# Performance work log

Hardware: AMD Instinct MI355X
Metric: run time of the kernel (lower is better)

The kernel has to match this reference:

```python
import jax, jax.numpy as jnp
import numpy as np

D_MODEL, NUM_HEADS, ROPE_DIM = 256, 8, 16
B_GRAPHS, N_MAX = 16, 512


def _make_batch():
    # ragged graph sizes between 256 and 512 atoms; contiguous, sorted ids
    sizes = np.array([256 + (i * 256) // 15 for i in range(B_GRAPHS)], dtype=np.int64)
    return np.repeat(np.arange(B_GRAPHS), sizes)  # total N = 6137


def setup_inputs() -> dict:
    key = jax.random.key(0)
    ks = jax.random.split(key, 6)
    batch_np = _make_batch()
    N = int(batch_np.shape[0])
    x = jax.random.normal(ks[0], (N, D_MODEL), jnp.float32)
    pos = jax.random.normal(ks[1], (N, 3), jnp.float32) * 3.0
    W_qkv = jax.random.normal(ks[2], (D_MODEL, 3 * D_MODEL), jnp.float32) / np.sqrt(D_MODEL).astype(np.float32)
    W_out = jax.random.normal(ks[3], (D_MODEL, D_MODEL), jnp.float32) / np.sqrt(D_MODEL).astype(np.float32)
    rope_freqs = jax.random.normal(ks[4], (ROPE_DIM,), jnp.float32) * 0.1
    W_rope = jax.random.normal(ks[5], (ROPE_DIM, NUM_HEADS), jnp.float32) / np.sqrt(ROPE_DIM).astype(np.float32)
    gamma = jnp.ones((D_MODEL,), jnp.float32)
    beta = jnp.zeros((D_MODEL,), jnp.float32)
    return {"x": x, "pos": pos, "batch": jnp.asarray(batch_np, jnp.int32),
            "W_qkv": W_qkv, "W_out": W_out, "rope_freqs": rope_freqs,
            "W_rope": W_rope, "gamma": gamma, "beta": beta,
            "B": B_GRAPHS, "n_max": N_MAX}


def _forward(x, pos, W_qkv, W_out, rope_freqs, W_rope, gamma, beta, batch, B, n_max):
    N, d = x.shape
    H = W_rope.shape[1]
    hd = d // H
    scale = hd ** -0.5
    # pad ragged graphs to [B, n_max] via vectorized scatter (batch is sorted)
    sizes = jax.ops.segment_sum(jnp.ones((N,), jnp.int32), batch, num_segments=B)
    offsets = jnp.concatenate([jnp.zeros((1,), jnp.int32), jnp.cumsum(sizes)[:-1].astype(jnp.int32)])
    pidx = jnp.arange(N, dtype=jnp.int32) - offsets[batch]  # position within graph
    x_pad = jnp.zeros((B, n_max, d), x.dtype).at[batch, pidx].set(x)
    pos_pad = jnp.zeros((B, n_max, 3), pos.dtype).at[batch, pidx].set(pos)
    pad = jnp.ones((B, n_max), bool).at[batch, pidx].set(False)  # True = padding
    # multi-head self-attention on scalar channel
    qkv = x_pad @ W_qkv  # [B, n, 3d]
    q, k, v = jnp.split(qkv, 3, axis=-1)
    heads = lambda t: t.reshape(B, n_max, H, hd).transpose(0, 2, 1, 3)  # [B,H,n,hd]
    q, k, v = heads(q), heads(k), heads(v)
    logits = jnp.einsum('bhid,bhjd->bhij', q, k) * scale
    # Euclidean RoPE distance bias: rope_proj(cos(|omega| * ||r_i - r_j||))
    diff = pos_pad[:, :, None, :] - pos_pad[:, None, :, :]  # [B,n,n,3]
    sq = jnp.sum(diff * diff, axis=-1)
    dist = jnp.where(sq > 0, jnp.sqrt(jnp.where(sq > 0, sq, 1.0)), 0.0)  # safe norm
    fourier = jnp.cos(dist[..., None] * jnp.abs(rope_freqs))  # [B,n,n,r]
    bias = jnp.einsum('bijr,rh->bhij', fourier, W_rope)
    pair_pad = (pad[:, :, None] | pad[:, None, :])[:, None]  # [B,1,n,n]
    bias = jnp.where(pair_pad, 0.0, bias)
    logits = jnp.where(pad[:, None, None, :], -1e9, logits + bias)
    attn = jax.nn.softmax(logits, axis=-1)
    out = jnp.einsum('bhij,bhjd->bhid', attn, v)
    out = out.transpose(0, 2, 1, 3).reshape(B, n_max, d) @ W_out
    out_flat = out[batch, pidx]  # gather back to flat node list
    # residual + LayerNorm (eps = 1e-5)
    y = x + out_flat
    mu = jnp.mean(y, axis=-1, keepdims=True)
    var = jnp.mean((y - mu) ** 2, axis=-1, keepdims=True)
    return gamma * (y - mu) * jax.lax.rsqrt(var + 1e-5) + beta


def reference(x, pos, batch, W_qkv, W_out, rope_freqs, W_rope, gamma, beta, B, n_max):
    return _forward(x, pos, W_qkv, W_out, rope_freqs, W_rope, gamma, beta, batch, B, n_max)
```

## Files before the change

### kernel.cpp

```cpp
#include <hip/hip_runtime.h>
#include <hip/hip_bf16.h>

typedef __hip_bfloat16 bf16;
typedef short bf16x8 __attribute__((ext_vector_type(8)));
typedef float f32x4 __attribute__((ext_vector_type(4)));

#define NGRAPH 16
#define QSCALE 0.17677669529663687f
#define VT_LD 8192

struct __align__(16) bf8x { bf16 v[8]; };

__device__ __forceinline__ float b2f(bf16 v) { return __bfloat162float(v); }

__device__ __forceinline__ bf16x8 ldcvt8(const float* p) {
  float4 u = *(const float4*)p, v = *(const float4*)(p + 4);
  __align__(16) bf16 tmp[8];
  tmp[0] = __float2bfloat16(u.x); tmp[1] = __float2bfloat16(u.y);
  tmp[2] = __float2bfloat16(u.z); tmp[3] = __float2bfloat16(u.w);
  tmp[4] = __float2bfloat16(v.x); tmp[5] = __float2bfloat16(v.y);
  tmp[6] = __float2bfloat16(v.z); tmp[7] = __float2bfloat16(v.w);
  return *(const bf16x8*)tmp;
}

__global__ __launch_bounds__(256) void k_pre(const float* __restrict__ Wqkv,
                                             const float* __restrict__ Wout,
                                             const int* __restrict__ batch,
                                             const float* __restrict__ freqs,
                                             const float* __restrict__ Wrope,
                                             bf16* __restrict__ Wqkv_t,
                                             bf16* __restrict__ Wout_t,
                                             float* __restrict__ Tblg,
                                             int* __restrict__ offs, int N) {
  __shared__ float ld[64][65];
  int bid = blockIdx.x, t = threadIdx.x;
  int c = t & 63, r0 = t >> 6;
  if (bid < 48) {
    int k0 = (bid & 3) * 64, n0 = (bid >> 2) * 64;
    #pragma unroll
    for (int r = r0; r < 64; r += 4) ld[r][c] = Wqkv[(size_t)(k0 + r) * 768 + n0 + c];
    __syncthreads();
    #pragma unroll
    for (int r = r0; r < 64; r += 4)
      Wqkv_t[(size_t)(n0 + r) * 256 + k0 + c] = __float2bfloat16(ld[c][r]);
  } else if (bid < 64) {
    int b2 = bid - 48;
    int k0 = (b2 & 3) * 64, n0 = (b2 >> 2) * 64;
    #pragma unroll
    for (int r = r0; r < 64; r += 4) ld[r][c] = Wout[(size_t)(k0 + r) * 256 + n0 + c];
    __syncthreads();
    #pragma unroll
    for (int r = r0; r < 64; r += 4)
      Wout_t[(size_t)(n0 + r) * 256 + k0 + c] = __float2bfloat16(ld[c][r]);
  } else if (bid == 64) {
    for (int i = t; i < N; i += 256) {
      if (i == 0) { offs[0] = 0; offs[NGRAPH] = N; }
      else if (batch[i] != batch[i - 1]) offs[batch[i]] = i;
    }
  } else {
    int i = (bid - 65) * 256 + t;
    if (i < 384) {
      float d = i * 0.125f;
      float a[8];
      #pragma unroll
      for (int h = 0; h < 8; ++h) a[h] = 0.f;
      #pragma unroll
      for (int r = 0; r < 16; ++r) {
        float cv = __cosf(d * fabsf(freqs[r]));
        #pragma unroll
        for (int h = 0; h < 8; ++h) a[h] += cv * Wrope[r * 8 + h];
      }
      #pragma unroll
      for (int h = 0; h < 8; ++h) Tblg[i * 8 + h] = a[h];
    }
  }
}

__global__ __launch_bounds__(256) void k_gemm(const float* __restrict__ x,
                                              const bf16* __restrict__ Wqkv_t,
                                              const int* __restrict__ batch,
                                              const int* __restrict__ offs,
                                              bf16* __restrict__ QKVb,
                                              bf16* __restrict__ VT, int N) {
  __shared__ float tr[64][33];
  __shared__ int rowcol[32];
  int t = threadIdx.x;
  int w = t >> 6, l = t & 63, fr = l & 15, fq = l >> 4;
  int rh = w & 1, ch = w >> 1;
  int m0 = blockIdx.x * 32, n0 = blockIdx.y * 64;
  if (t < 32) {
    int m = m0 + t; if (m > N - 1) m = N - 1;
    int b = batch[m];
    rowcol[t] = b * 512 + (m - offs[b]);
  }
  int arow = m0 + rh * 16 + fr; if (arow > N - 1) arow = N - 1;
  bf16x8 af[8];
  #pragma unroll
  for (int kt = 0; kt < 8; ++kt)
    af[kt] = ldcvt8(x + (size_t)arow * 256 + kt * 32 + fq * 8);
  #pragma unroll
  for (int p = 0; p < 3; ++p) {
    f32x4 acc[2];
    #pragma unroll
    for (int nt = 0; nt < 2; ++nt) {
      acc[nt] = (f32x4){0.f, 0.f, 0.f, 0.f};
      int brow = p * 256 + n0 + ch * 32 + nt * 16 + fr;
      #pragma unroll
      for (int kt = 0; kt < 8; ++kt) {
        bf16x8 bf_ = *(const bf16x8*)(Wqkv_t + (size_t)brow * 256 + kt * 32 + fq * 8);
        acc[nt] = __builtin_amdgcn_mfma_f32_16x16x32_bf16(af[kt], bf_, acc[nt], 0, 0, 0);
      }
    }
    float sc = (p == 0) ? QSCALE : 1.f;
    #pragma unroll
    for (int nt = 0; nt < 2; ++nt) {
      int col = p * 256 + n0 + ch * 32 + nt * 16 + fr;
      #pragma unroll
      for (int rr = 0; rr < 4; ++rr) {
        int m = m0 + rh * 16 + fq * 4 + rr;
        if (m < N) QKVb[(size_t)m * 768 + col] = __float2bfloat16(acc[nt][rr] * sc);
      }
    }
    if (p == 2) {
      #pragma unroll
      for (int nt = 0; nt < 2; ++nt)
        #pragma unroll
        for (int rr = 0; rr < 4; ++rr)
          tr[ch * 32 + nt * 16 + fr][rh * 16 + fq * 4 + rr] = acc[nt][rr];
      __syncthreads();
      int c = t >> 2, rr0 = (t & 3) * 8;
      int dg = n0 + c;
      #pragma unroll
      for (int i = 0; i < 8; ++i) {
        int r = rr0 + i;
        VT[(size_t)dg * VT_LD + rowcol[r]] = __float2bfloat16(tr[c][r]);
      }
    }
  }
}

__global__ __launch_bounds__(256) void k_attn(const float* __restrict__ pos,
                                              const float* __restrict__ Tblg,
                                              const bf16* __restrict__ QKVb,
                                              const bf16* __restrict__ VT,
                                              const int* __restrict__ offs,
                                              float* __restrict__ Op,
                                              float* __restrict__ lp, int N, int JC) {
  __shared__ __align__(16) float Tgf[384][8];
  __shared__ __align__(16) bf16 Sbf[2][8][64][8];
  __shared__ __align__(16) bf16 Pt[4][16][40];
  int b = blockIdx.y, jc = blockIdx.z;
  int off = offs[b], n = offs[b + 1] - off;
  int q0 = blockIdx.x * 16;
  if (q0 >= n) return;
  int t = threadIdx.x, w = t >> 6, l = t & 63, fr = l & 15, fq = l >> 4;

  {
    float4* dst = (float4*)&Tgf[0][0];
    const float4* src = (const float4*)Tblg;
    #pragma unroll
    for (int i = t; i < 768; i += 256) dst[i] = src[i];
  }

  int h0 = w, h1 = w + 4;
  const bf16* Kb0 = QKVb + (size_t)off * 768 + 256 + h0 * 32 + fq * 8;
  const bf16* Kb1 = QKVb + (size_t)off * 768 + 256 + h1 * 32 + fq * 8;
  const bf16* Vb0 = VT + (size_t)(h0 * 32 + fr) * VT_LD + b * 512 + fq * 8;
  const bf16* Vb1 = VT + (size_t)(h1 * 32 + fr) * VT_LD + b * 512 + fq * 8;
  int qrow = q0 + fr; bool qv = qrow < n;
  size_t qoff = (size_t)(qv ? off + qrow : off) * 768 + fq * 8;
  bf16x8 aq[2];
  aq[0] = *(const bf16x8*)(QKVb + qoff + h0 * 32);
  aq[1] = *(const bf16x8*)(QKVb + qoff + h1 * 32);
  if (!qv) { aq[0] = (bf16x8){0,0,0,0,0,0,0,0}; aq[1] = aq[0]; }

  int bq = t >> 5, bj = t & 31;
  float qpx[2], qpy[2], qpz[2]; bool bqv[2];
  #pragma unroll
  for (int e = 0; e < 2; ++e) {
    int qq = q0 + bq + 8 * e; bqv[e] = qq < n;
    int a = (bqv[e] ? off + qq : off) * 3;
    qpx[e] = pos[a]; qpy[e] = pos[a + 1]; qpz[e] = pos[a + 2];
  }

  f32x4 Oa[2][2];
  Oa[0][0] = (f32x4){0.f,0.f,0.f,0.f}; Oa[0][1] = Oa[0][0];
  Oa[1][0] = Oa[0][0];                 Oa[1][1] = Oa[0][0];
  float lacc[2][4] = {{0.f,0.f,0.f,0.f},{0.f,0.f,0.f,0.f}};
  int jtiles = (n + 31) >> 5;
  int jt0 = (jtiles * jc) / JC, jt1 = (jtiles * (jc + 1)) / JC;

  auto produce = [&](int JT, int BUF) {
    int jg = JT * 32 + bj; bool vj = jg < n;
    int a = (vj ? off + jg : off) * 3;
    float jx = pos[a], jy = pos[a + 1], jz = pos[a + 2];
    #pragma unroll
    for (int e = 0; e < 2; ++e) {
      int q = bq + 8 * e;
      int L = (q >> 2) * 16 + (bj & 15);
      int k = (bj >> 4) * 4 + (q & 3);
      if (vj && bqv[e]) {
        float dx = qpx[e] - jx, dy = qpy[e] - jy, dz = qpz[e] - jz;
        float d = sqrtf(dx * dx + dy * dy + dz * dz);
        float fi = d * 8.0f;
        int i = (int)fi; if (i > 382) i = 382;
        float fr2 = fi - (float)i;
        const float* tp = &Tgf[i][0];
        float4 a0 = *(const float4*)tp,       a1 = *(const float4*)(tp + 4);
        float4 c0 = *(const float4*)(tp + 8), c1 = *(const float4*)(tp + 12);
        Sbf[BUF][0][L][k] = __float2bfloat16(a0.x + fr2 * (c0.x - a0.x));
        Sbf[BUF][1][L][k] = __float2bfloat16(a0.y + fr2 * (c0.y - a0.y));
        Sbf[BUF][2][L][k] = __float2bfloat16(a0.z + fr2 * (c0.z - a0.z));
        Sbf[BUF][3][L][k] = __float2bfloat16(a0.w + fr2 * (c0.w - a0.w));
        Sbf[BUF][4][L][k] = __float2bfloat16(a1.x + fr2 * (c1.x - a1.x));
        Sbf[BUF][5][L][k] = __float2bfloat16(a1.y + fr2 * (c1.y - a1.y));
        Sbf[BUF][6][L][k] = __float2bfloat16(a1.z + fr2 * (c1.z - a1.z));
        Sbf[BUF][7][L][k] = __float2bfloat16(a1.w + fr2 * (c1.w - a1.w));
      } else {
        bf16 s = __float2bfloat16(vj ? 0.f : -1e30f);
        #pragma unroll
        for (int h = 0; h < 8; ++h) Sbf[BUF][h][L][k] = s;
      }
    }
  };

  bf16x8 ck[2][2], cv[2][2];
  auto loadt = [&](int JT) {
    int k0 = JT * 32 + fr, k1 = k0 + 16;
    size_t r0 = (size_t)((k0 < n) ? k0 : 0) * 768;
    size_t r1 = (size_t)((k1 < n) ? k1 : 0) * 768;
    ck[0][0] = *(const bf16x8*)(Kb0 + r0); ck[0][1] = *(const bf16x8*)(Kb0 + r1);
    ck[1][0] = *(const bf16x8*)(Kb1 + r0); ck[1][1] = *(const bf16x8*)(Kb1 + r1);
    cv[0][0] = *(const bf16x8*)(Vb0 + JT * 32);
    cv[0][1] = *(const bf16x8*)(Vb0 + (size_t)16 * VT_LD + JT * 32);
    cv[1][0] = *(const bf16x8*)(Vb1 + JT * 32);
    cv[1][1] = *(const bf16x8*)(Vb1 + (size_t)16 * VT_LD + JT * 32);
  };

  __syncthreads();
  produce(jt0, 0);
  __syncthreads();
  for (int jt = jt0; jt < jt1; ++jt) {
    int par = (jt - jt0) & 1;
    loadt(jt);
    if (jt + 1 < jt1) produce(jt + 1, par ^ 1);
    #pragma unroll
    for (int hh = 0; hh < 2; ++hh) {
      int h = w + 4 * hh;
      f32x4 z = {0.f, 0.f, 0.f, 0.f};
      f32x4 S0 = __builtin_amdgcn_mfma_f32_16x16x32_bf16(aq[hh], ck[hh][0], z, 0, 0, 0);
      f32x4 S1 = __builtin_amdgcn_mfma_f32_16x16x32_bf16(aq[hh], ck[hh][1], z, 0, 0, 0);
      bf8x bb = *(const bf8x*)&Sbf[par][h][l][0];
      #pragma unroll
      for (int k = 0; k < 8; ++k) {
        int jti = k >> 2, rr = k & 3;
        float s = (jti ? S1[rr] : S0[rr]) + b2f(bb.v[k]);
        float p = __expf(s);
        lacc[hh][rr] += p;
        Pt[w][fq * 4 + rr][jti * 16 + fr] = __float2bfloat16(p);
      }
      bf16x8 ap = *(const bf16x8*)&Pt[w][fr][fq * 8];
      Oa[hh][0] = __builtin_amdgcn_mfma_f32_16x16x32_bf16(ap, cv[hh][0], Oa[hh][0], 0, 0, 0);
      Oa[hh][1] = __builtin_amdgcn_mfma_f32_16x16x32_bf16(ap, cv[hh][1], Oa[hh][1], 0, 0, 0);
    }
    __syncthreads();
  }
  #pragma unroll
  for (int hh = 0; hh < 2; ++hh)
    #pragma unroll
    for (int rr = 0; rr < 4; ++rr) {
      #pragma unroll
      for (int m2 = 1; m2 <= 8; m2 <<= 1) lacc[hh][rr] += __shfl_xor(lacc[hh][rr], m2);
    }
  float* Opc = Op + (size_t)jc * N * 256;
  float* lpc = lp + (size_t)jc * N * 8;
  #pragma unroll
  for (int hh = 0; hh < 2; ++hh) {
    int h = w + 4 * hh;
    #pragma unroll
    for (int rr = 0; rr < 4; ++rr) {
      int row = q0 + fq * 4 + rr;
      if (row < n) {
        #pragma unroll
        for (int dh = 0; dh < 2; ++dh)
          Opc[(size_t)(off + row) * 256 + h * 32 + dh * 16 + fr] = Oa[hh][dh][rr];
        if (fr == 0) lpc[(size_t)(off + row) * 8 + h] = lacc[hh][rr];
      }
    }
  }
}

__global__ __launch_bounds__(256) void k_out_ln(const float* __restrict__ Op,
                                                const float* __restrict__ lp,
                                                const bf16* __restrict__ Bt,
                                                const float* __restrict__ x,
                                                const float* __restrict__ gamma,
                                                const float* __restrict__ beta,
                                                float* __restrict__ out, int M, int JC) {
  __shared__ float ps[4][16], pss[4][16];
  int t = threadIdx.x, w = t >> 6, l = t & 63, fr = l & 15, fq = l >> 4;
  int m0 = blockIdx.x * 16;
  int arow = m0 + fr; if (arow > M - 1) arow = M - 1;
  float linv[8];
  {
    float ls[8] = {0.f,0.f,0.f,0.f,0.f,0.f,0.f,0.f};
    for (int c = 0; c < JC; ++c) {
      const float* p = lp + ((size_t)c * M + arow) * 8;
      float4 a0 = *(const float4*)p, a1 = *(const float4*)(p + 4);
      ls[0] += a0.x; ls[1] += a0.y; ls[2] += a0.z; ls[3] += a0.w;
      ls[4] += a1.x; ls[5] += a1.y; ls[6] += a1.z; ls[7] += a1.w;
    }
    #pragma unroll
    for (int h = 0; h < 8; ++h) linv[h] = 1.f / ls[h];
  }
  bf16x8 af[8];
  #pragma unroll
  for (int kt = 0; kt < 8; ++kt) {
    size_t o = (size_t)arow * 256 + kt * 32 + fq * 8;
    float s0 = 0.f, s1 = 0.f, s2 = 0.f, s3 = 0.f, s4 = 0.f, s5 = 0.f, s6 = 0.f, s7 = 0.f;
    for (int c = 0; c < JC; ++c) {
      const float* p = Op + (size_t)c * M * 256 + o;
      float4 u = *(const float4*)p, v = *(const float4*)(p + 4);
      s0 += u.x; s1 += u.y; s2 += u.z; s3 += u.w;
      s4 += v.x; s5 += v.y; s6 += v.z; s7 += v.w;
    }
    float li = linv[kt];
    __align__(16) bf16 tmp[8];
    tmp[0] = __float2bfloat16(s0 * li); tmp[1] = __float2bfloat16(s1 * li);
    tmp[2] = __float2bfloat16(s2 * li); tmp[3] = __float2bfloat16(s3 * li);
    tmp[4] = __float2bfloat16(s4 * li); tmp[5] = __float2bfloat16(s5 * li);
    tmp[6] = __float2bfloat16(s6 * li); tmp[7] = __float2bfloat16(s7 * li);
    af[kt] = *(const bf16x8*)tmp;
  }
  f32x4 acc[4];
  #pragma unroll
  for (int nt = 0; nt < 4; ++nt) {
    acc[nt] = (f32x4){0.f, 0.f, 0.f, 0.f};
    int brow = w * 64 + nt * 16 + fr;
    #pragma unroll
    for (int kt = 0; kt < 8; ++kt) {
      bf16x8 bf_ = *(const bf16x8*)(Bt + (size_t)brow * 256 + kt * 32 + fq * 8);
      acc[nt] = __builtin_amdgcn_mfma_f32_16x16x32_bf16(af[kt], bf_, acc[nt], 0, 0, 0);
    }
  }
  float y[4][4];
  #pragma unroll
  for (int rr = 0; rr < 4; ++rr) {
    int row = m0 + fq * 4 + rr;
    int rc = (row < M) ? row : (M - 1);
    float s = 0.f, ss = 0.f;
    #pragma unroll
    for (int nt = 0; nt < 4; ++nt) {
      float v = acc[nt][rr] + x[(size_t)rc * 256 + w * 64 + nt * 16 + fr];
      y[rr][nt] = v; s += v; ss += v * v;
    }
    #pragma unroll
    for (int m2 = 1; m2 <= 8; m2 <<= 1) { s += __shfl_xor(s, m2); ss += __shfl_xor(ss, m2); }
    if (fr == 0) { ps[w][fq * 4 + rr] = s; pss[w][fq * 4 + rr] = ss; }
  }
  __syncthreads();
  #pragma unroll
  for (int rr = 0; rr < 4; ++rr) {
    int row = m0 + fq * 4 + rr;
    int ri = fq * 4 + rr;
    float s = ps[0][ri] + ps[1][ri] + ps[2][ri] + ps[3][ri];
    float ss = pss[0][ri] + pss[1][ri] + pss[2][ri] + pss[3][ri];
    float mean = s * (1.f / 256.f);
    float var = ss * (1.f / 256.f) - mean * mean;
    float rstd = rsqrtf(var + 1e-5f);
    if (row < M) {
      #pragma unroll
      for (int nt = 0; nt < 4; ++nt) {
        int col = w * 64 + nt * 16 + fr;
        out[(size_t)row * 256 + col] = gamma[col] * (y[rr][nt] - mean) * rstd + beta[col];
      }
    }
  }
}

extern "C" void kernel_launch(void* const* d_in, const int* in_sizes, int n_in,
                              void* d_out, int out_size, void* d_ws, size_t ws_size,
                              hipStream_t stream) {
  (void)n_in; (void)out_size;
  const float* x     = (const float*)d_in[0];
  const float* pos   = (const float*)d_in[1];
  const int*   batch = (const int*)d_in[2];
  const float* Wqkv  = (const float*)d_in[3];
  const float* Wout  = (const float*)d_in[4];
  const float* freqs = (const float*)d_in[5];
  const float* Wrope = (const float*)d_in[6];
  const float* gamma = (const float*)d_in[7];
  const float* beta  = (const float*)d_in[8];
  float* out = (float*)d_out;

  int N = in_sizes[0] / 256;

  int JC = (ws_size >= (size_t)41 * 1024 * 1024) ? 4 : 2;

  char* base = (char*)d_ws;
  int*   offs   = (int*)base;
  bf16*  QKVb   = (bf16*)(base + 1024);
  bf16*  VT     = (bf16*)(base + 9427456);
  bf16*  Wqkv_t = (bf16*)(base + 13621760);
  bf16*  Wout_t = (bf16*)(base + 14014976);
  float* Tblg   = (float*)(base + 14146048);
  float* Op     = (float*)(base + 14158336);
  float* lp     = (float*)(base + 14158336 + (size_t)JC * N * 1024);

  int MBm = (N + 31) / 32;
  k_pre<<<67, 256, 0, stream>>>(Wqkv, Wout, batch, freqs, Wrope, Wqkv_t, Wout_t, Tblg, offs, N);
  k_gemm<<<dim3(MBm, 4), 256, 0, stream>>>(x, Wqkv_t, batch, offs, QKVb, VT, N);
  k_attn<<<dim3(32, NGRAPH, JC), 256, 0, stream>>>(pos, Tblg, QKVb, VT, offs, Op, lp, N, JC);
  k_out_ln<<<(N + 15) / 16, 256, 0, stream>>>(Op, lp, Wout_t, x, gamma, beta, out, N, JC);
}
```

Measured before the change: 182.8 us.

## Compute RoPE distance bias per lane in MFMA layout, removing shared staging and barriers

The cooperative producer stage that wrote a double-buffered bf16 bias tile to shared memory is removed, along with the per-tile __syncthreads. Each lane now computes the interpolated distance bias itself, directly in the MFMA accumulator layout and for its own head pair. It does this from graph positions cached once in shared memory and a packed bf16 head-pair lookup table. This cuts LDS traffic and synchronisation but duplicates some distance and sqrt work across waves, since each of the 4 waves recomputes distances for the same query/key pairs.

```diff
diff --git a/kernel.cpp b/kernel.cpp
--- a/kernel.cpp
+++ b/kernel.cpp
@@ -8,10 +8,6 @@
 #define NGRAPH 16
 #define QSCALE 0.17677669529663687f
 #define VT_LD 8192
-
-struct __align__(16) bf8x { bf16 v[8]; };
-
-__device__ __forceinline__ float b2f(bf16 v) { return __bfloat162float(v); }
 
 __device__ __forceinline__ bf16x8 ldcvt8(const float* p) {
   float4 u = *(const float4*)p, v = *(const float4*)(p + 4);
@@ -146,8 +142,8 @@
                                               const int* __restrict__ offs,
                                               float* __restrict__ Op,
                                               float* __restrict__ lp, int N, int JC) {
-  __shared__ __align__(16) float Tgf[384][8];
-  __shared__ __align__(16) bf16 Sbf[2][8][64][8];
+  __shared__ unsigned int T2u[1536];
+  __shared__ float px[512], py[512], pz[512];
   __shared__ __align__(16) bf16 Pt[4][16][40];
   int b = blockIdx.y, jc = blockIdx.z;
   int off = offs[b], n = offs[b + 1] - off;
@@ -155,11 +151,18 @@
   if (q0 >= n) return;
   int t = threadIdx.x, w = t >> 6, l = t & 63, fr = l & 15, fq = l >> 4;
 
-  {
-    float4* dst = (float4*)&Tgf[0][0];
-    const float4* src = (const float4*)Tblg;
-    #pragma unroll
-    for (int i = t; i < 768; i += 256) dst[i] = src[i];
+  for (int e = t; e < 1536; e += 256) {
+    int i = e >> 2, hp = e & 3;
+    bf16 blo = __float2bfloat16(Tblg[i * 8 + hp]);
+    bf16 bhi = __float2bfloat16(Tblg[i * 8 + hp + 4]);
+    unsigned short ulo = *(unsigned short*)&blo, uhi = *(unsigned short*)&bhi;
+    T2u[e] = (unsigned)ulo | ((unsigned)uhi << 16);
+  }
+  int n3 = n * 3;
+  for (int idx = t; idx < n3; idx += 256) {
+    float v = pos[(size_t)off * 3 + idx];
+    int slot = idx / 3, c = idx - slot * 3;
+    if (c == 0) px[slot] = v; else if (c == 1) py[slot] = v; else pz[slot] = v;
   }
 
   int h0 = w, h1 = w + 4;
@@ -174,13 +177,13 @@
   aq[1] = *(const bf16x8*)(QKVb + qoff + h1 * 32);
   if (!qv) { aq[0] = (bf16x8){0,0,0,0,0,0,0,0}; aq[1] = aq[0]; }
 
-  int bq = t >> 5, bj = t & 31;
-  float qpx[2], qpy[2], qpz[2]; bool bqv[2];
-  #pragma unroll
-  for (int e = 0; e < 2; ++e) {
-    int qq = q0 + bq + 8 * e; bqv[e] = qq < n;
-    int a = (bqv[e] ? off + qq : off) * 3;
-    qpx[e] = pos[a]; qpy[e] = pos[a + 1]; qpz[e] = pos[a + 2];
+  __syncthreads();
+
+  float qx[4], qy[4], qz[4];
+  #pragma unroll
+  for (int rr = 0; rr < 4; ++rr) {
+    int qq = q0 + fq * 4 + rr; if (qq >= n) qq = n - 1;
+    qx[rr] = px[qq]; qy[rr] = py[qq]; qz[rr] = pz[qq];
   }
 
   f32x4 Oa[2][2];
@@ -190,81 +193,67 @@
   int jtiles = (n + 31) >> 5;
   int jt0 = (jtiles * jc) / JC, jt1 = (jtiles * (jc + 1)) / JC;
 
-  auto produce = [&](int JT, int BUF) {
-    int jg = JT * 32 + bj; bool vj = jg < n;
-    int a = (vj ? off + jg : off) * 3;
-    float jx = pos[a], jy = pos[a + 1], jz = pos[a + 2];
-    #pragma unroll
-    for (int e = 0; e < 2; ++e) {
-      int q = bq + 8 * e;
-      int L = (q >> 2) * 16 + (bj & 15);
-      int k = (bj >> 4) * 4 + (q & 3);
-      if (vj && bqv[e]) {
-        float dx = qpx[e] - jx, dy = qpy[e] - jy, dz = qpz[e] - jz;
-        float d = sqrtf(dx * dx + dy * dy + dz * dz);
-        float fi = d * 8.0f;
-        int i = (int)fi; if (i > 382) i = 382;
-        float fr2 = fi - (float)i;
-        const float* tp = &Tgf[i][0];
-        float4 a0 = *(const float4*)tp,       a1 = *(const float4*)(tp + 4);
-        float4 c0 = *(const float4*)(tp + 8), c1 = *(const float4*)(tp + 12);
-        Sbf[BUF][0][L][k] = __float2bfloat16(a0.x + fr2 * (c0.x - a0.x));
-        Sbf[BUF][1][L][k] = __float2bfloat16(a0.y + fr2 * (c0.y - a0.y));
-        Sbf[BUF][2][L][k] = __float2bfloat16(a0.z + fr2 * (c0.z - a0.z));
-        Sbf[BUF][3][L][k] = __float2bfloat16(a0.w + fr2 * (c0.w - a0.w));
-        Sbf[BUF][4][L][k] = __float2bfloat16(a1.x + fr2 * (c1.x - a1.x));
-        Sbf[BUF][5][L][k] = __float2bfloat16(a1.y + fr2 * (c1.y - a1.y));
-        Sbf[BUF][6][L][k] = __float2bfloat16(a1.z + fr2 * (c1.z - a1.z));
-        Sbf[BUF][7][L][k] = __float2bfloat16(a1.w + fr2 * (c1.w - a1.w));
-      } else {
-        bf16 s = __float2bfloat16(vj ? 0.f : -1e30f);
-        #pragma unroll
-        for (int h = 0; h < 8; ++h) Sbf[BUF][h][L][k] = s;
-      }
-    }
-  };
-
-  bf16x8 ck[2][2], cv[2][2];
-  auto loadt = [&](int JT) {
-    int k0 = JT * 32 + fr, k1 = k0 + 16;
+  for (int jt = jt0; jt < jt1; ++jt) {
+    int k0 = jt * 32 + fr, k1 = k0 + 16;
     size_t r0 = (size_t)((k0 < n) ? k0 : 0) * 768;
     size_t r1 = (size_t)((k1 < n) ? k1 : 0) * 768;
-    ck[0][0] = *(const bf16x8*)(Kb0 + r0); ck[0][1] = *(const bf16x8*)(Kb0 + r1);
-    ck[1][0] = *(const bf16x8*)(Kb1 + r0); ck[1][1] = *(const bf16x8*)(Kb1 + r1);
-    cv[0][0] = *(const bf16x8*)(Vb0 + JT * 32);
-    cv[0][1] = *(const bf16x8*)(Vb0 + (size_t)16 * VT_LD + JT * 32);
-    cv[1][0] = *(const bf16x8*)(Vb1 + JT * 32);
-    cv[1][1] = *(const bf16x8*)(Vb1 + (size_t)16 * VT_LD + JT * 32);
-  };
-
-  __syncthreads();
-  produce(jt0, 0);
-  __syncthreads();
-  for (int jt = jt0; jt < jt1; ++jt) {
-    int par = (jt - jt0) & 1;
-    loadt(jt);
-    if (jt + 1 < jt1) produce(jt + 1, par ^ 1);
+    bf16x8 ck00 = *(const bf16x8*)(Kb0 + r0), ck01 = *(const bf16x8*)(Kb0 + r1);
+    bf16x8 ck10 = *(const bf16x8*)(Kb1 + r0), ck11 = *(const bf16x8*)(Kb1 + r1);
+    bf16x8 cv00 = *(const bf16x8*)(Vb0 + jt * 32);
+    bf16x8 cv01 = *(const bf16x8*)(Vb0 + (size_t)16 * VT_LD + jt * 32);
+    bf16x8 cv10 = *(const bf16x8*)(Vb1 + jt * 32);
+    bf16x8 cv11 = *(const bf16x8*)(Vb1 + (size_t)16 * VT_LD + jt * 32);
+
+    bool vj0 = k0 < n, vj1 = k1 < n;
+    int js0 = vj0 ? k0 : 0, js1 = vj1 ? k1 : 0;
+    float jx0 = px[js0], jy0 = py[js0], jz0 = pz[js0];
+    float jx1 = px[js1], jy1 = py[js1], jz1 = pz[js1];
+    float bias[2][2][4];
+    #pragma unroll
+    for (int rr = 0; rr < 4; ++rr) {
+      {
+        float dx = qx[rr] - jx0, dy = qy[rr] - jy0, dz = qz[rr] - jz0;
+        float fi = sqrtf(dx * dx + dy * dy + dz * dz) * 8.0f;
+        int i = (int)fi; if (i > 382) i = 382;
+        float f2 = fi - (float)i;
+        unsigned ua = T2u[i * 4 + w], ub = T2u[i * 4 + 4 + w];
+        float la = __uint_as_float(ua << 16), ha = __uint_as_float(ua & 0xffff0000u);
+        float lb = __uint_as_float(ub << 16), hb = __uint_as_float(ub & 0xffff0000u);
+        bias[0][0][rr] = vj0 ? (la + f2 * (lb - la)) : -1e30f;
+        bias[0][1][rr] = vj0 ? (ha + f2 * (hb - ha)) : -1e30f;
+      }
+      {
+        float dx = qx[rr] - jx1, dy = qy[rr] - jy1, dz = qz[rr] - jz1;
+        float fi = sqrtf(dx * dx + dy * dy + dz * dz) * 8.0f;
+        int i = (int)fi; if (i > 382) i = 382;
+        float f2 = fi - (float)i;
+        unsigned ua = T2u[i * 4 + w], ub = T2u[i * 4 + 4 + w];
+        float la = __uint_as_float(ua << 16), ha = __uint_as_float(ua & 0xffff0000u);
+        float lb = __uint_as_float(ub << 16), hb = __uint_as_float(ub & 0xffff0000u);
+        bias[1][0][rr] = vj1 ? (la + f2 * (lb - la)) : -1e30f;
+        bias[1][1][rr] = vj1 ? (ha + f2 * (hb - ha)) : -1e30f;
+      }
+    }
+
     #pragma unroll
     for (int hh = 0; hh < 2; ++hh) {
-      int h = w + 4 * hh;
       f32x4 z = {0.f, 0.f, 0.f, 0.f};
-      f32x4 S0 = __builtin_amdgcn_mfma_f32_16x16x32_bf16(aq[hh], ck[hh][0], z, 0, 0, 0);
-      f32x4 S1 = __builtin_amdgcn_mfma_f32_16x16x32_bf16(aq[hh], ck[hh][1], z, 0, 0, 0);
-      bf8x bb = *(const bf8x*)&Sbf[par][h][l][0];
+      f32x4 S0 = __builtin_amdgcn_mfma_f32_16x16x32_bf16(aq[hh], hh ? ck10 : ck00, z, 0, 0, 0);
+      f32x4 S1 = __builtin_amdgcn_mfma_f32_16x16x32_bf16(aq[hh], hh ? ck11 : ck01, z, 0, 0, 0);
       #pragma unroll
       for (int k = 0; k < 8; ++k) {
         int jti = k >> 2, rr = k & 3;
-        float s = (jti ? S1[rr] : S0[rr]) + b2f(bb.v[k]);
+        float s = (jti ? S1[rr] : S0[rr]) + bias[jti][hh][rr];
         float p = __expf(s);
         lacc[hh][rr] += p;
         Pt[w][fq * 4 + rr][jti * 16 + fr] = __float2bfloat16(p);
       }
       bf16x8 ap = *(const bf16x8*)&Pt[w][fr][fq * 8];
-      Oa[hh][0] = __builtin_amdgcn_mfma_f32_16x16x32_bf16(ap, cv[hh][0], Oa[hh][0], 0, 0, 0);
-      Oa[hh][1] = __builtin_amdgcn_mfma_f32_16x16x32_bf16(ap, cv[hh][1], Oa[hh][1], 0, 0, 0);
-    }
-    __syncthreads();
-  }
+      Oa[hh][0] = __builtin_amdgcn_mfma_f32_16x16x32_bf16(ap, hh ? cv10 : cv00, Oa[hh][0], 0, 0, 0);
+      Oa[hh][1] = __builtin_amdgcn_mfma_f32_16x16x32_bf16(ap, hh ? cv11 : cv01, Oa[hh][1], 0, 0, 0);
+    }
+  }
+
   #pragma unroll
   for (int hh = 0; hh < 2; ++hh)
     #pragma unroll
```

Measured after the change: 180.3 us. No clear change (-1.4%).
